# Kernel optimization log

Measured on AMD Instinct MI355X. Metric: run time of the kernel, lower is better.

## Reference

```python
import jax, jax.numpy as jnp
import numpy as np

B, N, H, R, L = 32, 512, 768, 5, 2
FF = 2 * H  # ffn expansion = hidden_size * 2
LN_EPS = 1e-5


def layer_norm(x, g, b):
    mu = jnp.mean(x, axis=-1, keepdims=True)
    var = jnp.mean(jnp.square(x - mu), axis=-1, keepdims=True)
    return (x - mu) * jax.lax.rsqrt(var + LN_EPS) * g + b


def setup_inputs() -> dict:
    key = jax.random.key(0)
    ks = jax.random.split(key, 20)
    s = 1.0 / np.sqrt(H)
    inp = {
        'node_embeddings': jax.random.normal(ks[0], (B, N, H), jnp.float32),
        'relation_graph': jax.random.uniform(ks[1], (B, R, N, N), jnp.float32),
        # stacked per-layer params (leading dim = L layers)
        'rel_W': jax.random.normal(ks[2], (L, R, H, H), jnp.float32) * s,
        'rel_b': jax.random.normal(ks[3], (L, R, H), jnp.float32) * s,
        'gate_W': jax.random.normal(ks[4], (L, H, R), jnp.float32) * s,
        'gate_b': jax.random.normal(ks[5], (L, R), jnp.float32) * s,
        'out_W': jax.random.normal(ks[6], (L, H, H), jnp.float32) * s,
        'out_b': jax.random.normal(ks[7], (L, H), jnp.float32) * s,
        'ln1_g': jnp.ones((L, H), jnp.float32),
        'ln1_b': jnp.zeros((L, H), jnp.float32),
        'ffn_W1': jax.random.normal(ks[8], (L, H, FF), jnp.float32) * s,
        'ffn_b1': jax.random.normal(ks[9], (L, FF), jnp.float32) * s,
        'ffn_W2': jax.random.normal(ks[10], (L, FF, H), jnp.float32) * (1.0 / np.sqrt(FF)),
        'ffn_b2': jax.random.normal(ks[11], (L, H), jnp.float32) * s,
        'ln2_g': jnp.ones((L, H), jnp.float32),
        'ln2_b': jnp.zeros((L, H), jnp.float32),
    }
    return inp


def reference(node_embeddings, relation_graph, rel_W, rel_b, gate_W, gate_b,
              out_W, out_b, ln1_g, ln1_b, ffn_W1, ffn_b1, ffn_W2, ffn_b2,
              ln2_g, ln2_b):
    adj = relation_graph.astype(jnp.float32)            # [B,R,N,N]
    deg = jnp.clip(jnp.sum(adj, axis=-1, keepdims=True), 1.0)  # [B,R,N,1]
    x = node_embeddings
    rw_collect = []
    for l in range(rel_W.shape[0]):  # small fixed layer count
        # per-relation degree-normalized aggregation + linear + relu
        agg = jnp.einsum('brnm,bmh->brnh', adj, x) / deg           # [B,R,N,H]
        msg = jax.nn.relu(jnp.einsum('brnh,rhd->brnd', agg, rel_W[l])
                          + rel_b[l][None, :, None, :])            # [B,R,N,H]
        # softmax gate over relations from mean-pooled nodes
        pooled = jnp.mean(x, axis=1)                                # [B,H]
        logits = pooled @ gate_W[l] + gate_b[l]                     # [B,R]
        w = jax.nn.softmax(logits, axis=-1)
        merged = jnp.einsum('brnd,br->bnd', msg, w)                 # [B,N,H]
        merged = merged @ out_W[l] + out_b[l]                       # dropout=identity (eval)
        hidden = layer_norm(x + merged, ln1_g[l], ln1_b[l])
        ff = jax.nn.relu(hidden @ ffn_W1[l] + ffn_b1[l]) @ ffn_W2[l] + ffn_b2[l]
        x = layer_norm(hidden + ff, ln2_g[l], ln2_b[l])
        rw_collect.append(jnp.mean(w, axis=0))
    relation_weights_stat = jnp.mean(jnp.stack(rw_collect, axis=0), axis=0)  # [R]
    return x, relation_weights_stat
```

## Files before the change

### kernel.cpp

```cpp
#include <hip/hip_runtime.h>
#include <hip/hip_bf16.h>
#include <math.h>

#define Bdim 32
#define Ndim 512
#define Hdim 768
#define Rdim 5
#define Ldim 2
#define FFdim 1536
#define LN_EPS 1e-5f

typedef __attribute__((ext_vector_type(8))) __bf16 bf16x8;
typedef __attribute__((ext_vector_type(8))) unsigned short ushort8;
typedef __attribute__((ext_vector_type(4))) float f32x4;

__device__ __forceinline__ unsigned short f2bf(float f) {
  union { float f; unsigned int u; } x;
  x.f = f;
  unsigned int u = x.u;
  return (unsigned short)((u + 0x7FFFu + ((u >> 16) & 1u)) >> 16);
}

__device__ __forceinline__ void gload_lds16(const unsigned short* g, unsigned short* l) {
  __builtin_amdgcn_global_load_lds(
      (const __attribute__((address_space(1))) void*)g,
      (__attribute__((address_space(3))) void*)l, 16, 0, 0);
}

template <int EPI, bool OUT_BF16, int NSEG>
__global__ __launch_bounds__(256) void mfma_gemm(
    const unsigned short* __restrict__ A, long sA, long sA2, int lda,
    const unsigned short* __restrict__ Bt, long sB, int ldb,
    void* __restrict__ Cp, long sC, int ldc,
    int segK, long segA, long segB,
    const float* __restrict__ bias,
    const float* __restrict__ resid,
    const float* __restrict__ wv) {
  __shared__ __align__(16) unsigned short As[128 * 32];
  __shared__ __align__(16) unsigned short Bs[128 * 32];

  const int zb = blockIdx.z;
  const int zlo = zb & 31;
  const int zhi = zb >> 5;
  const int row0 = blockIdx.y * 128;
  const int col0 = blockIdx.x * 128;
  const int tid = threadIdx.x;
  const int wid = tid >> 6;
  const int lane = tid & 63;
  const int mq = (wid & 1) * 64;
  const int nq = (wid >> 1) * 64;
  const int lr = lane & 15;
  const int lk = (lane >> 4) * 8;

  const int c0 = wid * 2;
  const int srow0 = c0 * 16 + (lane >> 2);
  const int se = (lane & 3) * 8;

  const unsigned short* Abase = A + (long)zlo * sA + (long)zhi * sA2;
  const unsigned short* Bbase = Bt + (long)zlo * sB;
  unsigned short* Al0 = As + c0 * 512;
  unsigned short* Al1 = As + c0 * 512 + 512;
  unsigned short* Bl0 = Bs + c0 * 512;
  unsigned short* Bl1 = Bs + c0 * 512 + 512;

  f32x4 acc[4][4];
  f32x4 acc2[4][4];
#pragma unroll
  for (int i = 0; i < 4; i++)
#pragma unroll
    for (int j = 0; j < 4; j++) {
      acc[i][j] = (f32x4){0.f, 0.f, 0.f, 0.f};
      if (EPI == 1) acc2[i][j] = (f32x4){0.f, 0.f, 0.f, 0.f};
    }

  for (int seg = 0; seg < NSEG; seg++) {
    const unsigned short* Ag0 = Abase + (long)seg * segA + (long)(row0 + srow0) * lda + se;
    const unsigned short* Ag1 = Ag0 + (long)16 * lda;
    const unsigned short* Bg0 = Bbase + (long)seg * segB + (long)(col0 + srow0) * ldb + se;
    const unsigned short* Bg1 = Bg0 + (long)16 * ldb;

    for (int k0 = 0; k0 < segK; k0 += 32) {
      gload_lds16(Ag0 + k0, Al0);
      gload_lds16(Ag1 + k0, Al1);
      gload_lds16(Bg0 + k0, Bl0);
      gload_lds16(Bg1 + k0, Bl1);
      __syncthreads();

      bf16x8 af[4], bfr[4];
#pragma unroll
      for (int i = 0; i < 4; i++) af[i] = *(const bf16x8*)&As[(mq + i * 16 + lr) * 32 + lk];
#pragma unroll
      for (int j = 0; j < 4; j++) bfr[j] = *(const bf16x8*)&Bs[(nq + j * 16 + lr) * 32 + lk];
#pragma unroll
      for (int i = 0; i < 4; i++)
#pragma unroll
        for (int j = 0; j < 4; j++)
          acc[i][j] = __builtin_amdgcn_mfma_f32_16x16x32_bf16(af[i], bfr[j], acc[i][j], 0, 0, 0);
      __syncthreads();
    }

    if (EPI == 1) {
      const float wval = wv[(row0 >> 9) * Rdim + seg];
#pragma unroll
      for (int j = 0; j < 4; j++) {
        const float bj = bias[seg * Hdim + col0 + nq + j * 16 + lr];
#pragma unroll
        for (int i = 0; i < 4; i++)
#pragma unroll
          for (int rr = 0; rr < 4; rr++) {
            acc2[i][j][rr] += wval * fmaxf(acc[i][j][rr] + bj, 0.f);
            acc[i][j][rr] = 0.f;
          }
      }
    }
  }

  float bvals[4];
  if (EPI == 2 || EPI == 3) {
#pragma unroll
    for (int j = 0; j < 4; j++) bvals[j] = bias[col0 + nq + j * 16 + lr];
  }

  float* Cf = (float*)Cp;
  unsigned short* Ch = (unsigned short*)Cp;
  const long Coff = (long)zb * sC;

#pragma unroll
  for (int i = 0; i < 4; i++) {
#pragma unroll
    for (int r = 0; r < 4; r++) {
      const int grow = row0 + mq + i * 16 + (lane >> 4) * 4 + r;
#pragma unroll
      for (int j = 0; j < 4; j++) {
        const int gcol = col0 + nq + j * 16 + lr;
        const long cidx = Coff + (long)grow * ldc + gcol;
        float v;
        if (EPI == 1) v = acc2[i][j][r];
        else v = acc[i][j][r];
        if (EPI == 2) v += bvals[j] + resid[cidx];
        if (EPI == 3) v = fmaxf(v + bvals[j], 0.f);
        if (OUT_BF16) Ch[cidx] = f2bf(v);
        else Cf[cidx] = v;
      }
    }
  }
}

__global__ __launch_bounds__(256) void transpose_cvt(
    const float* __restrict__ in, unsigned short* __restrict__ out, int R_, int C_) {
  __shared__ float t[32][33];
  const int z = blockIdx.z;
  const float* ib = in + (long)z * R_ * C_;
  unsigned short* ob = out + (long)z * R_ * C_;
  const int r0 = blockIdx.y * 32, c0 = blockIdx.x * 32;
  const int tx = threadIdx.x & 31, ty = threadIdx.x >> 5;
#pragma unroll
  for (int i = 0; i < 4; i++)
    t[ty + i * 8][tx] = ib[(long)(r0 + ty + i * 8) * C_ + c0 + tx];
  __syncthreads();
#pragma unroll
  for (int i = 0; i < 4; i++)
    ob[(long)(c0 + ty + i * 8) * R_ + r0 + tx] = f2bf(t[tx][ty + i * 8]);
}

__global__ __launch_bounds__(256) void norm_adj_kernel(const float* __restrict__ adj,
                                                       unsigned short* __restrict__ out,
                                                       long total_rows) {
  const long w = ((long)blockIdx.x * 256 + threadIdx.x) >> 6;
  const int lane = threadIdx.x & 63;
  if (w >= total_rows) return;
  const float* row = adj + w * Ndim;
  float4 f0 = *(const float4*)(row + lane * 8);
  float4 f1 = *(const float4*)(row + lane * 8 + 4);
  float s = f0.x + f0.y + f0.z + f0.w + f1.x + f1.y + f1.z + f1.w;
#pragma unroll
  for (int off = 32; off; off >>= 1) s += __shfl_xor(s, off, 64);
  const float inv = 1.0f / fmaxf(s, 1.0f);
  ushort8 o = {f2bf(f0.x * inv), f2bf(f0.y * inv), f2bf(f0.z * inv), f2bf(f0.w * inv),
               f2bf(f1.x * inv), f2bf(f1.y * inv), f2bf(f1.z * inv), f2bf(f1.w * inv)};
  *(ushort8*)&out[w * Ndim + lane * 8] = o;
}

__global__ __launch_bounds__(256) void pool_kernel(const float* __restrict__ x,
                                                   float* __restrict__ part) {
  const int ch = blockIdx.x, b = blockIdx.y, t = threadIdx.x;
  const float* xb = x + ((long)b * Ndim + ch * 64) * Hdim;
  float s0 = 0.f, s1 = 0.f, s2 = 0.f;
  for (int n = 0; n < 64; n++) {
    const float* r = xb + (long)n * Hdim;
    s0 += r[t]; s1 += r[t + 256]; s2 += r[t + 512];
  }
  float* p = part + ((long)b * 8 + ch) * Hdim;
  p[t] = s0; p[t + 256] = s1; p[t + 512] = s2;
}

__global__ void gate_kernel(const float* __restrict__ part,
                            const float* __restrict__ gW,
                            const float* __restrict__ gb,
                            float* __restrict__ w_out) {
  __shared__ float pooled[Hdim];
  __shared__ float logits[Rdim];
  const int b = blockIdx.x;
  const int h = threadIdx.x;
  float s = 0.f;
#pragma unroll
  for (int c = 0; c < 8; c++) s += part[((long)b * 8 + c) * Hdim + h];
  pooled[h] = s * (1.0f / Ndim);
  __syncthreads();
  if (h < Rdim) {
    float acc = gb[h];
    for (int k = 0; k < Hdim; k++) acc += pooled[k] * gW[k * Rdim + h];
    logits[h] = acc;
  }
  __syncthreads();
  if (h == 0) {
    float mx = -1e30f;
    for (int r = 0; r < Rdim; r++) mx = fmaxf(mx, logits[r]);
    float e[Rdim];
    float se = 0.f;
    for (int r = 0; r < Rdim; r++) { e[r] = expf(logits[r] - mx); se += e[r]; }
    for (int r = 0; r < Rdim; r++) w_out[b * Rdim + r] = e[r] / se;
  }
}

__global__ __launch_bounds__(256) void ln_kernel(
    const float* __restrict__ X,
    const float* __restrict__ g, const float* __restrict__ bb,
    float* __restrict__ out, unsigned short* __restrict__ out_bf) {
  __shared__ float red[8];
  const long base = (long)blockIdx.x * Hdim;
  const int t = threadIdx.x;
  float v0 = X[base + t];
  float v1 = X[base + t + 256];
  float v2 = X[base + t + 512];
  float s = v0 + v1 + v2;
  float ss = v0 * v0 + v1 * v1 + v2 * v2;
#pragma unroll
  for (int off = 32; off > 0; off >>= 1) {
    s += __shfl_down(s, off, 64);
    ss += __shfl_down(ss, off, 64);
  }
  const int wid = t >> 6;
  if ((t & 63) == 0) { red[wid] = s; red[4 + wid] = ss; }
  __syncthreads();
  s = red[0] + red[1] + red[2] + red[3];
  ss = red[4] + red[5] + red[6] + red[7];
  const float mu = s * (1.0f / Hdim);
  const float var = ss * (1.0f / Hdim) - mu * mu;
  const float inv = rsqrtf(var + LN_EPS);
  const float o0 = (v0 - mu) * inv * g[t] + bb[t];
  const float o1 = (v1 - mu) * inv * g[t + 256] + bb[t + 256];
  const float o2 = (v2 - mu) * inv * g[t + 512] + bb[t + 512];
  out[base + t] = o0;
  out[base + t + 256] = o1;
  out[base + t + 512] = o2;
  if (out_bf) {
    out_bf[base + t] = f2bf(o0);
    out_bf[base + t + 256] = f2bf(o1);
    out_bf[base + t + 512] = f2bf(o2);
  }
}

__global__ void stat_kernel(const float* __restrict__ w_buf, float* __restrict__ out) {
  const int r = threadIdx.x;
  if (r < Rdim) {
    float s = 0.f;
    for (int l = 0; l < Ldim; l++)
      for (int b = 0; b < Bdim; b++) s += w_buf[l * Bdim * Rdim + b * Rdim + r];
    out[r] = s * (1.0f / (Ldim * Bdim));
  }
}

extern "C" void kernel_launch(void* const* d_in, const int* in_sizes, int n_in,
                              void* d_out, int out_size, void* d_ws, size_t ws_size,
                              hipStream_t stream) {
  const float* node = (const float*)d_in[0];
  const float* adj  = (const float*)d_in[1];
  const float* relW = (const float*)d_in[2];
  const float* relb = (const float*)d_in[3];
  const float* gateW = (const float*)d_in[4];
  const float* gateb = (const float*)d_in[5];
  const float* outW = (const float*)d_in[6];
  const float* outb = (const float*)d_in[7];
  const float* ln1g = (const float*)d_in[8];
  const float* ln1b = (const float*)d_in[9];
  const float* fW1 = (const float*)d_in[10];
  const float* fb1 = (const float*)d_in[11];
  const float* fW2 = (const float*)d_in[12];
  const float* fb2 = (const float*)d_in[13];
  const float* ln2g = (const float*)d_in[14];
  const float* ln2b = (const float*)d_in[15];

  const long BNH = (long)Bdim * Ndim * Hdim;
  const long BRNN = (long)Bdim * Rdim * Ndim * Ndim;
  float* xout = (float*)d_out;
  float* stat = xout + BNH;

  float* ws = (float*)d_ws;
  float* hidden = ws;
  float* tmp    = ws + BNH;
  unsigned short* agg_all = (unsigned short*)(ws + 2 * BNH);
  unsigned short* xT_bf = agg_all + Rdim * BNH;
  unsigned short* merged_bf = xT_bf + BNH;
  unsigned short* adjn_bf = merged_bf + BNH;
  unsigned short* relWT = adjn_bf + BRNN;
  unsigned short* outWT = relWT + (long)Ldim * Rdim * Hdim * Hdim;
  unsigned short* W1T = outWT + (long)Ldim * Hdim * Hdim;
  unsigned short* W2T = W1T + (long)Ldim * Hdim * FFdim;
  float* w_buf = (float*)(W2T + (long)Ldim * FFdim * Hdim);
  float* part = w_buf + Ldim * Bdim * Rdim;
  unsigned short* hidden_bf = xT_bf;
  unsigned short* ffh_bf = (unsigned short*)tmp;
  float* tmp2 = (float*)agg_all;

  {
    const long rows = (long)Bdim * Rdim * Ndim;
    norm_adj_kernel<<<(int)(rows / 4), 256, 0, stream>>>(adj, adjn_bf, rows);
  }
  transpose_cvt<<<dim3(Hdim / 32, Hdim / 32, Ldim * Rdim), 256, 0, stream>>>(relW, relWT, Hdim, Hdim);
  transpose_cvt<<<dim3(Hdim / 32, Hdim / 32, Ldim), 256, 0, stream>>>(outW, outWT, Hdim, Hdim);
  transpose_cvt<<<dim3(FFdim / 32, Hdim / 32, Ldim), 256, 0, stream>>>(fW1, W1T, Hdim, FFdim);
  transpose_cvt<<<dim3(Hdim / 32, FFdim / 32, Ldim), 256, 0, stream>>>(fW2, W2T, FFdim, Hdim);

  for (int l = 0; l < Ldim; l++) {
    const float* xin = (l == 0) ? node : xout;

    pool_kernel<<<dim3(8, Bdim), 256, 0, stream>>>(xin, part);
    gate_kernel<<<Bdim, Hdim, 0, stream>>>(
        part, gateW + (long)l * Hdim * Rdim, gateb + (long)l * Rdim,
        w_buf + (long)l * Bdim * Rdim);

    transpose_cvt<<<dim3(Hdim / 32, Ndim / 32, Bdim), 256, 0, stream>>>(xin, xT_bf, Ndim, Hdim);

    mfma_gemm<0, true, 1><<<dim3(Hdim / 128, Ndim / 128, Bdim * Rdim), 256, 0, stream>>>(
        adjn_bf, (long)Rdim * Ndim * Ndim, (long)Ndim * Ndim, Ndim,
        xT_bf, (long)Hdim * Ndim, Ndim,
        agg_all, (long)Ndim * Hdim, Hdim,
        Ndim, 0, 0, nullptr, nullptr, nullptr);

    mfma_gemm<1, true, Rdim><<<dim3(Hdim / 128, (Bdim * Ndim) / 128, 1), 256, 0, stream>>>(
        agg_all, 0, 0, Hdim,
        relWT + (long)l * Rdim * Hdim * Hdim, 0, Hdim,
        merged_bf, 0, Hdim,
        Hdim, BNH, (long)Hdim * Hdim,
        relb + (long)l * Rdim * Hdim, nullptr,
        w_buf + (long)l * Bdim * Rdim);

    mfma_gemm<2, false, 1><<<dim3(Hdim / 128, (Bdim * Ndim) / 128, 1), 256, 0, stream>>>(
        merged_bf, 0, 0, Hdim,
        outWT + (long)l * Hdim * Hdim, 0, Hdim,
        tmp, 0, Hdim,
        Hdim, 0, 0,
        outb + (long)l * Hdim, xin, nullptr);

    ln_kernel<<<Bdim * Ndim, 256, 0, stream>>>(
        tmp, ln1g + (long)l * Hdim, ln1b + (long)l * Hdim, hidden, hidden_bf);

    mfma_gemm<3, true, 1><<<dim3(FFdim / 128, (Bdim * Ndim) / 128, 1), 256, 0, stream>>>(
        hidden_bf, 0, 0, Hdim,
        W1T + (long)l * Hdim * FFdim, 0, Hdim,
        ffh_bf, 0, FFdim,
        Hdim, 0, 0,
        fb1 + (long)l * FFdim, nullptr, nullptr);

    mfma_gemm<2, false, 1><<<dim3(Hdim / 128, (Bdim * Ndim) / 128, 1), 256, 0, stream>>>(
        ffh_bf, 0, 0, FFdim,
        W2T + (long)l * FFdim * Hdim, 0, FFdim,
        tmp2, 0, Hdim,
        FFdim, 0, 0,
        fb2 + (long)l * Hdim, hidden, nullptr);

    ln_kernel<<<Bdim * Ndim, 256, 0, stream>>>(
        tmp2, ln2g + (long)l * Hdim, ln2b + (long)l * Hdim, xout, nullptr);
  }

  stat_kernel<<<1, 64, 0, stream>>>(w_buf, stat);
}
```

Before: 1.688 ms.

## Double-buffer LDS tiles in MFMA GEMM and remap blocks across XCDs

The GEMM main loop now uses two LDS buffers, so the global-to-LDS load of the next K-step is issued while MFMAs run on the current one, with one barrier per step instead of two. The per-segment loop is flattened into a single step sequence, and the relation fold is triggered by a counter. Block indices are also remapped so that consecutive logical tiles land on the same XCD, which should improve L2 reuse. LDS use doubles, which may lower occupancy.

Measured after the change: 1.493 ms. -11.6%, faster.

```diff
diff --git a/kernel.cpp b/kernel.cpp
--- a/kernel.cpp
+++ b/kernel.cpp
@@ -36,14 +36,29 @@
     const float* __restrict__ bias,
     const float* __restrict__ resid,
     const float* __restrict__ wv) {
-  __shared__ __align__(16) unsigned short As[128 * 32];
-  __shared__ __align__(16) unsigned short Bs[128 * 32];
-
-  const int zb = blockIdx.z;
+  __shared__ __align__(16) unsigned short As0[128 * 32];
+  __shared__ __align__(16) unsigned short Bs0[128 * 32];
+  __shared__ __align__(16) unsigned short As1[128 * 32];
+  __shared__ __align__(16) unsigned short Bs1[128 * 32];
+
+  const int gx = gridDim.x, gy = gridDim.y;
+  int lin = blockIdx.x + gx * (blockIdx.y + gy * blockIdx.z);
+  {
+    const int total = gx * gy * gridDim.z;
+    const int q = total >> 3, r8 = total & 7;
+    const int xcd = lin & 7, slot = lin >> 3;
+    lin = (xcd < r8) ? (xcd * (q + 1) + slot)
+                     : (r8 * (q + 1) + (xcd - r8) * q + slot);
+  }
+  const int bx = lin % gx;
+  const int t2 = lin / gx;
+  const int by = t2 % gy;
+  const int zb = t2 / gy;
+
   const int zlo = zb & 31;
   const int zhi = zb >> 5;
-  const int row0 = blockIdx.y * 128;
-  const int col0 = blockIdx.x * 128;
+  const int row0 = by * 128;
+  const int col0 = bx * 128;
   const int tid = threadIdx.x;
   const int wid = tid >> 6;
   const int lane = tid & 63;
@@ -56,12 +71,11 @@
   const int srow0 = c0 * 16 + (lane >> 2);
   const int se = (lane & 3) * 8;
 
-  const unsigned short* Abase = A + (long)zlo * sA + (long)zhi * sA2;
-  const unsigned short* Bbase = Bt + (long)zlo * sB;
-  unsigned short* Al0 = As + c0 * 512;
-  unsigned short* Al1 = As + c0 * 512 + 512;
-  unsigned short* Bl0 = Bs + c0 * 512;
-  unsigned short* Bl1 = Bs + c0 * 512 + 512;
+  const unsigned short* Ag0 =
+      A + (long)zlo * sA + (long)zhi * sA2 + (long)(row0 + srow0) * lda + se;
+  const unsigned short* Ag1 = Ag0 + (long)16 * lda;
+  const unsigned short* Bg0 = Bt + (long)zlo * sB + (long)(col0 + srow0) * ldb + se;
+  const unsigned short* Bg1 = Bg0 + (long)16 * ldb;
 
   f32x4 acc[4][4];
   f32x4 acc2[4][4];
@@ -73,45 +87,64 @@
       if (EPI == 1) acc2[i][j] = (f32x4){0.f, 0.f, 0.f, 0.f};
     }
 
-  for (int seg = 0; seg < NSEG; seg++) {
-    const unsigned short* Ag0 = Abase + (long)seg * segA + (long)(row0 + srow0) * lda + se;
-    const unsigned short* Ag1 = Ag0 + (long)16 * lda;
-    const unsigned short* Bg0 = Bbase + (long)seg * segB + (long)(col0 + srow0) * ldb + se;
-    const unsigned short* Bg1 = Bg0 + (long)16 * ldb;
-
-    for (int k0 = 0; k0 < segK; k0 += 32) {
-      gload_lds16(Ag0 + k0, Al0);
-      gload_lds16(Ag1 + k0, Al1);
-      gload_lds16(Bg0 + k0, Bl0);
-      gload_lds16(Bg1 + k0, Bl1);
+  const int spseg = segK >> 5;
+  const int nsteps = NSEG * spseg;
+  int sseg = 0, sk = 0;
+
+  auto stage = [&](unsigned short* Asl, unsigned short* Bsl) {
+    const long ao = (long)sseg * segA + sk;
+    const long bo = (long)sseg * segB + sk;
+    gload_lds16(Ag0 + ao, Asl + c0 * 512);
+    gload_lds16(Ag1 + ao, Asl + c0 * 512 + 512);
+    gload_lds16(Bg0 + bo, Bsl + c0 * 512);
+    gload_lds16(Bg1 + bo, Bsl + c0 * 512 + 512);
+    sk += 32;
+    if (sk == segK) { sk = 0; sseg++; }
+  };
+
+  auto compute = [&](const unsigned short* Asb, const unsigned short* Bsb) {
+    bf16x8 af[4], bfr[4];
+#pragma unroll
+    for (int i = 0; i < 4; i++) af[i] = *(const bf16x8*)&Asb[(mq + i * 16 + lr) * 32 + lk];
+#pragma unroll
+    for (int j = 0; j < 4; j++) bfr[j] = *(const bf16x8*)&Bsb[(nq + j * 16 + lr) * 32 + lk];
+#pragma unroll
+    for (int i = 0; i < 4; i++)
+#pragma unroll
+      for (int j = 0; j < 4; j++)
+        acc[i][j] = __builtin_amdgcn_mfma_f32_16x16x32_bf16(af[i], bfr[j], acc[i][j], 0, 0, 0);
+  };
+
+  int cnt = 0, cseg = 0;
+  auto fold = [&]() {
+    const float wval = wv[(row0 >> 9) * Rdim + cseg];
+#pragma unroll
+    for (int j = 0; j < 4; j++) {
+      const float bj = bias[cseg * Hdim + col0 + nq + j * 16 + lr];
+#pragma unroll
+      for (int i = 0; i < 4; i++)
+#pragma unroll
+        for (int rr = 0; rr < 4; rr++) {
+          acc2[i][j][rr] += wval * fmaxf(acc[i][j][rr] + bj, 0.f);
+          acc[i][j][rr] = 0.f;
+        }
+    }
+    cseg++;
+  };
+
+  stage(As0, Bs0);
+  __syncthreads();
+
+  for (int s = 0; s < nsteps; s += 2) {
+    if (s + 1 < nsteps) stage(As1, Bs1);
+    compute(As0, Bs0);
+    if (EPI == 1 && ++cnt == spseg) { fold(); cnt = 0; }
+    __syncthreads();
+    if (s + 1 < nsteps) {
+      if (s + 2 < nsteps) stage(As0, Bs0);
+      compute(As1, Bs1);
+      if (EPI == 1 && ++cnt == spseg) { fold(); cnt = 0; }
       __syncthreads();
-
-      bf16x8 af[4], bfr[4];
-#pragma unroll
-      for (int i = 0; i < 4; i++) af[i] = *(const bf16x8*)&As[(mq + i * 16 + lr) * 32 + lk];
-#pragma unroll
-      for (int j = 0; j < 4; j++) bfr[j] = *(const bf16x8*)&Bs[(nq + j * 16 + lr) * 32 + lk];
-#pragma unroll
-      for (int i = 0; i < 4; i++)
-#pragma unroll
-        for (int j = 0; j < 4; j++)
-          acc[i][j] = __builtin_amdgcn_mfma_f32_16x16x32_bf16(af[i], bfr[j], acc[i][j], 0, 0, 0);
-      __syncthreads();
-    }
-
-    if (EPI == 1) {
-      const float wval = wv[(row0 >> 9) * Rdim + seg];
-#pragma unroll
-      for (int j = 0; j < 4; j++) {
-        const float bj = bias[seg * Hdim + col0 + nq + j * 16 + lr];
-#pragma unroll
-        for (int i = 0; i < 4; i++)
-#pragma unroll
-          for (int rr = 0; rr < 4; rr++) {
-            acc2[i][j][rr] += wval * fmaxf(acc[i][j][rr] + bj, 0.f);
-            acc[i][j][rr] = 0.f;
-          }
-      }
     }
   }
 
```

## Rewrite MFMA GEMM with 256x128 tiles, double-buffered swizzled LDS, and XCD-aware block remap

Applied to the files above, without the earlier changes.

The bf16 MFMA GEMM moves from 128x128 tiles with K=32 and a single LDS buffer to 256x128 tiles with 512 threads, K=64 steps, and double-buffered LDS. Rows are XOR-swizzled to avoid bank conflicts. Global-to-LDS prefetch of the next stage overlaps with the MFMA work, using explicit waitcnt and barriers, and s_setprio raises priority around the MFMA bursts. Block indices are remapped so consecutive tiles land on the same XCD for better L2 reuse, and the per-segment bias and gate values are preloaded. The risks are higher register and LDS pressure (96KB of LDS per block) and fragile hand-written synchronization.

After: 1.654 ms. 1.02x faster.

```diff
diff --git a/kernel.cpp b/kernel.cpp
--- a/kernel.cpp
+++ b/kernel.cpp
@@ -28,7 +28,7 @@
 }
 
 template <int EPI, bool OUT_BF16, int NSEG>
-__global__ __launch_bounds__(256) void mfma_gemm(
+__global__ __launch_bounds__(512, 2) void mfma_gemm(
     const unsigned short* __restrict__ A, long sA, long sA2, int lda,
     const unsigned short* __restrict__ Bt, long sB, int ldb,
     void* __restrict__ Cp, long sC, int ldc,
@@ -36,35 +36,53 @@
     const float* __restrict__ bias,
     const float* __restrict__ resid,
     const float* __restrict__ wv) {
-  __shared__ __align__(16) unsigned short As[128 * 32];
-  __shared__ __align__(16) unsigned short Bs[128 * 32];
-
-  const int zb = blockIdx.z;
+  __shared__ __align__(16) unsigned short As[2 * 256 * 64];
+  __shared__ __align__(16) unsigned short Bs[2 * 128 * 64];
+
+  const int gx = gridDim.x, gy = gridDim.y;
+  int lin = blockIdx.x + gx * (blockIdx.y + gy * blockIdx.z);
+  {
+    const int total = gx * gy * gridDim.z;
+    const int q = total >> 3, r8 = total & 7;
+    const int xcd = lin & 7, slot = lin >> 3;
+    lin = (xcd < r8) ? (xcd * (q + 1) + slot)
+                     : (r8 * (q + 1) + (xcd - r8) * q + slot);
+  }
+  const int bx = lin % gx;
+  const int tv = lin / gx;
+  const int by = tv % gy;
+  const int zb = tv / gy;
+
   const int zlo = zb & 31;
   const int zhi = zb >> 5;
-  const int row0 = blockIdx.y * 128;
-  const int col0 = blockIdx.x * 128;
+  const int row0 = by * 256;
+  const int col0 = bx * 128;
   const int tid = threadIdx.x;
   const int wid = tid >> 6;
   const int lane = tid & 63;
-  const int mq = (wid & 1) * 64;
-  const int nq = (wid >> 1) * 64;
+  const int wr = wid >> 1;
+  const int wc = wid & 1;
   const int lr = lane & 15;
-  const int lk = (lane >> 4) * 8;
-
-  const int c0 = wid * 2;
-  const int srow0 = c0 * 16 + (lane >> 2);
-  const int se = (lane & 3) * 8;
+  const int lks = lane >> 4;
+
+  const int rl = lane >> 3;
+  const int cl = ((lane & 7) ^ rl) * 8;
 
   const unsigned short* Abase = A + (long)zlo * sA + (long)zhi * sA2;
   const unsigned short* Bbase = Bt + (long)zlo * sB;
-  unsigned short* Al0 = As + c0 * 512;
-  unsigned short* Al1 = As + c0 * 512 + 512;
-  unsigned short* Bl0 = Bs + c0 * 512;
-  unsigned short* Bl1 = Bs + c0 * 512 + 512;
-
-  f32x4 acc[4][4];
-  f32x4 acc2[4][4];
+
+  float pw[NSEG], pb[NSEG][4];
+  if (EPI == 1) {
+#pragma unroll
+    for (int s = 0; s < NSEG; s++) {
+      pw[s] = wv[(row0 >> 9) * Rdim + s];
+#pragma unroll
+      for (int fc = 0; fc < 4; fc++)
+        pb[s][fc] = bias[s * Hdim + col0 + wc * 64 + fc * 16 + lr];
+    }
+  }
+
+  f32x4 acc[4][4], acc2[4][4];
 #pragma unroll
   for (int i = 0; i < 4; i++)
 #pragma unroll
@@ -73,72 +91,134 @@
       if (EPI == 1) acc2[i][j] = (f32x4){0.f, 0.f, 0.f, 0.f};
     }
 
+  const int spt = segK >> 6;
+  const int T = NSEG * spt;
+  int aseg = 0, ak = 0, bseg = 0, bk = 0;
+
+  auto stageA = [&](int parity) {
+    const unsigned short* s0 = Abase + (long)aseg * segA + ak;
+#pragma unroll
+    for (int q = 0; q < 4; q++) {
+      const int ch = wid * 4 + q;
+      gload_lds16(s0 + (long)(row0 + ch * 8 + rl) * lda + cl,
+                  As + parity * 16384 + ch * 512);
+    }
+    ak += 64;
+    if (ak == segK) { ak = 0; aseg++; }
+  };
+  auto stageB = [&](int parity) {
+    const unsigned short* s0 = Bbase + (long)bseg * segB + bk;
+#pragma unroll
+    for (int q = 0; q < 2; q++) {
+      const int ch = wid * 2 + q;
+      gload_lds16(s0 + (long)(col0 + ch * 8 + rl) * ldb + cl,
+                  Bs + parity * 8192 + ch * 512);
+    }
+    bk += 64;
+    if (bk == segK) { bk = 0; bseg++; }
+  };
+
+  stageA(0);
+  stageB(0);
+  if (T > 1) stageB(1);
+
   for (int seg = 0; seg < NSEG; seg++) {
-    const unsigned short* Ag0 = Abase + (long)seg * segA + (long)(row0 + srow0) * lda + se;
-    const unsigned short* Ag1 = Ag0 + (long)16 * lda;
-    const unsigned short* Bg0 = Bbase + (long)seg * segB + (long)(col0 + srow0) * ldb + se;
-    const unsigned short* Bg1 = Bg0 + (long)16 * ldb;
-
-    for (int k0 = 0; k0 < segK; k0 += 32) {
-      gload_lds16(Ag0 + k0, Al0);
-      gload_lds16(Ag1 + k0, Al1);
-      gload_lds16(Bg0 + k0, Bl0);
-      gload_lds16(Bg1 + k0, Bl1);
-      __syncthreads();
-
-      bf16x8 af[4], bfr[4];
-#pragma unroll
-      for (int i = 0; i < 4; i++) af[i] = *(const bf16x8*)&As[(mq + i * 16 + lr) * 32 + lk];
-#pragma unroll
-      for (int j = 0; j < 4; j++) bfr[j] = *(const bf16x8*)&Bs[(nq + j * 16 + lr) * 32 + lk];
-#pragma unroll
-      for (int i = 0; i < 4; i++)
-#pragma unroll
-        for (int j = 0; j < 4; j++)
-          acc[i][j] = __builtin_amdgcn_mfma_f32_16x16x32_bf16(af[i], bfr[j], acc[i][j], 0, 0, 0);
-      __syncthreads();
-    }
-
+#pragma unroll 1
+    for (int kk = 0; kk < spt; kk++) {
+      const int t = seg * spt + kk;
+      const int par = t & 1;
+      if (t == T - 1) asm volatile("s_waitcnt vmcnt(0)" ::: "memory");
+      else            asm volatile("s_waitcnt vmcnt(2)" ::: "memory");
+      __builtin_amdgcn_s_barrier();
+
+      const unsigned short* Ab = As + par * 16384;
+      const unsigned short* Bb = Bs + par * 8192;
+
+      bf16x8 bfr[4][2], afr[2][2];
+#pragma unroll
+      for (int fc = 0; fc < 4; fc++)
+#pragma unroll
+        for (int ks = 0; ks < 2; ks++) {
+          const int r = wc * 64 + fc * 16 + lr;
+          bfr[fc][ks] = *(const bf16x8*)&Bb[r * 64 + (((ks * 4 + lks) ^ (r & 7)) << 3)];
+        }
+#pragma unroll
+      for (int fr = 0; fr < 2; fr++)
+#pragma unroll
+        for (int ks = 0; ks < 2; ks++) {
+          const int r = wr * 64 + fr * 16 + lr;
+          afr[fr][ks] = *(const bf16x8*)&Ab[r * 64 + (((ks * 4 + lks) ^ (r & 7)) << 3)];
+        }
+      if (t + 1 < T) stageA(par ^ 1);
+      asm volatile("s_waitcnt lgkmcnt(0)" ::: "memory");
+      __builtin_amdgcn_sched_barrier(0);
+      __builtin_amdgcn_s_setprio(1);
+#pragma unroll
+      for (int fr = 0; fr < 2; fr++)
+#pragma unroll
+        for (int fc = 0; fc < 4; fc++)
+#pragma unroll
+          for (int ks = 0; ks < 2; ks++)
+            acc[fr][fc] = __builtin_amdgcn_mfma_f32_16x16x32_bf16(
+                afr[fr][ks], bfr[fc][ks], acc[fr][fc], 0, 0, 0);
+      __builtin_amdgcn_s_setprio(0);
+      __builtin_amdgcn_s_barrier();
+
+#pragma unroll
+      for (int fr = 0; fr < 2; fr++)
+#pragma unroll
+        for (int ks = 0; ks < 2; ks++) {
+          const int r = wr * 64 + (fr + 2) * 16 + lr;
+          afr[fr][ks] = *(const bf16x8*)&Ab[r * 64 + (((ks * 4 + lks) ^ (r & 7)) << 3)];
+        }
+      if (t + 2 < T) stageB(par);
+      asm volatile("s_waitcnt lgkmcnt(0)" ::: "memory");
+      __builtin_amdgcn_sched_barrier(0);
+      __builtin_amdgcn_s_setprio(1);
+#pragma unroll
+      for (int fr = 0; fr < 2; fr++)
+#pragma unroll
+        for (int fc = 0; fc < 4; fc++)
+#pragma unroll
+          for (int ks = 0; ks < 2; ks++)
+            acc[fr + 2][fc] = __builtin_amdgcn_mfma_f32_16x16x32_bf16(
+                afr[fr][ks], bfr[fc][ks], acc[fr + 2][fc], 0, 0, 0);
+      __builtin_amdgcn_s_setprio(0);
+    }
     if (EPI == 1) {
-      const float wval = wv[(row0 >> 9) * Rdim + seg];
-#pragma unroll
-      for (int j = 0; j < 4; j++) {
-        const float bj = bias[seg * Hdim + col0 + nq + j * 16 + lr];
-#pragma unroll
-        for (int i = 0; i < 4; i++)
+#pragma unroll
+      for (int fr = 0; fr < 4; fr++)
+#pragma unroll
+        for (int fc = 0; fc < 4; fc++)
 #pragma unroll
           for (int rr = 0; rr < 4; rr++) {
-            acc2[i][j][rr] += wval * fmaxf(acc[i][j][rr] + bj, 0.f);
-            acc[i][j][rr] = 0.f;
+            acc2[fr][fc][rr] += pw[seg] * fmaxf(acc[fr][fc][rr] + pb[seg][fc], 0.f);
+            acc[fr][fc][rr] = 0.f;
           }
-      }
     }
   }
 
   float bvals[4];
   if (EPI == 2 || EPI == 3) {
 #pragma unroll
-    for (int j = 0; j < 4; j++) bvals[j] = bias[col0 + nq + j * 16 + lr];
-  }
-
+    for (int fc = 0; fc < 4; fc++) bvals[fc] = bias[col0 + wc * 64 + fc * 16 + lr];
+  }
   float* Cf = (float*)Cp;
   unsigned short* Ch = (unsigned short*)Cp;
   const long Coff = (long)zb * sC;
 
 #pragma unroll
-  for (int i = 0; i < 4; i++) {
-#pragma unroll
-    for (int r = 0; r < 4; r++) {
-      const int grow = row0 + mq + i * 16 + (lane >> 4) * 4 + r;
-#pragma unroll
-      for (int j = 0; j < 4; j++) {
-        const int gcol = col0 + nq + j * 16 + lr;
+  for (int fr = 0; fr < 4; fr++) {
+#pragma unroll
+    for (int rr = 0; rr < 4; rr++) {
+      const int grow = row0 + wr * 64 + fr * 16 + lks * 4 + rr;
+#pragma unroll
+      for (int fc = 0; fc < 4; fc++) {
+        const int gcol = col0 + wc * 64 + fc * 16 + lr;
         const long cidx = Coff + (long)grow * ldc + gcol;
-        float v;
-        if (EPI == 1) v = acc2[i][j][r];
-        else v = acc[i][j][r];
-        if (EPI == 2) v += bvals[j] + resid[cidx];
-        if (EPI == 3) v = fmaxf(v + bvals[j], 0.f);
+        float v = (EPI == 1) ? acc2[fr][fc][rr] : acc[fr][fc][rr];
+        if (EPI == 2) v += bvals[fc] + resid[cidx];
+        if (EPI == 3) v = fmaxf(v + bvals[fc], 0.f);
         if (OUT_BF16) Ch[cidx] = f2bf(v);
         else Cf[cidx] = v;
       }
@@ -332,13 +412,13 @@
 
     transpose_cvt<<<dim3(Hdim / 32, Ndim / 32, Bdim), 256, 0, stream>>>(xin, xT_bf, Ndim, Hdim);
 
-    mfma_gemm<0, true, 1><<<dim3(Hdim / 128, Ndim / 128, Bdim * Rdim), 256, 0, stream>>>(
+    mfma_gemm<0, true, 1><<<dim3(Hdim / 128, Ndim / 256, Bdim * Rdim), 512, 0, stream>>>(
         adjn_bf, (long)Rdim * Ndim * Ndim, (long)Ndim * Ndim, Ndim,
         xT_bf, (long)Hdim * Ndim, Ndim,
         agg_all, (long)Ndim * Hdim, Hdim,
         Ndim, 0, 0, nullptr, nullptr, nullptr);
 
-    mfma_gemm<1, true, Rdim><<<dim3(Hdim / 128, (Bdim * Ndim) / 128, 1), 256, 0, stream>>>(
+    mfma_gemm<1, true, Rdim><<<dim3(Hdim / 128, (Bdim * Ndim) / 256, 1), 512, 0, stream>>>(
         agg_all, 0, 0, Hdim,
         relWT + (long)l * Rdim * Hdim * Hdim, 0, Hdim,
         merged_bf, 0, Hdim,
@@ -346,7 +426,7 @@
         relb + (long)l * Rdim * Hdim, nullptr,
         w_buf + (long)l * Bdim * Rdim);
 
-    mfma_gemm<2, false, 1><<<dim3(Hdim / 128, (Bdim * Ndim) / 128, 1), 256, 0, stream>>>(
+    mfma_gemm<2, false, 1><<<dim3(Hdim / 128, (Bdim * Ndim) / 256, 1), 512, 0, stream>>>(
         merged_bf, 0, 0, Hdim,
         outWT + (long)l * Hdim * Hdim, 0, Hdim,
         tmp, 0, Hdim,
@@ -356,14 +436,14 @@
     ln_kernel<<<Bdim * Ndim, 256, 0, stream>>>(
         tmp, ln1g + (long)l * Hdim, ln1b + (long)l * Hdim, hidden, hidden_bf);
 
-    mfma_gemm<3, true, 1><<<dim3(FFdim / 128, (Bdim * Ndim) / 128, 1), 256, 0, stream>>>(
+    mfma_gemm<3, true, 1><<<dim3(FFdim / 128, (Bdim * Ndim) / 256, 1), 512, 0, stream>>>(
         hidden_bf, 0, 0, Hdim,
         W1T + (long)l * Hdim * FFdim, 0, Hdim,
         ffh_bf, 0, FFdim,
         Hdim, 0, 0,
         fb1 + (long)l * FFdim, nullptr, nullptr);
 
-    mfma_gemm<2, false, 1><<<dim3(Hdim / 128, (Bdim * Ndim) / 128, 1), 256, 0, stream>>>(
+    mfma_gemm<2, false, 1><<<dim3(Hdim / 128, (Bdim * Ndim) / 256, 1), 512, 0, stream>>>(
         ffh_bf, 0, 0, FFdim,
         W2T + (long)l * FFdim * Hdim, 0, FFdim,
         tmp2, 0, Hdim,
```
